# Kernel optimization log

Hardware: AMD Instinct MI355X
Metric: run time of the kernel (lower is better)

Reference implementation:

```python
import jax, jax.numpy as jnp
import numpy as np

NEG_SLOPE = 0.2
EPS = 1e-16  # PyG softmax denominator epsilon


def gatv2_layer(x, src, dst, W_l, W_r, att, bias, num_nodes, heads, out_dim, concat):
    # x: [N, F_in]; src/dst: [E] (self-loops already included)
    x_l = (x @ W_l).reshape(num_nodes, heads, out_dim)  # source transform
    x_r = (x @ W_r).reshape(num_nodes, heads, out_dim)  # target transform
    # GATv2 scoring: a^T LeakyReLU(x_l[j] + x_r[i])
    e = jax.nn.leaky_relu(x_l[src] + x_r[dst], NEG_SLOPE)       # [E, H, D]
    logits = jnp.einsum('ehd,hd->eh', e, att)                    # [E, H]
    # segment softmax over incoming edges of each target node
    m = jax.ops.segment_max(logits, dst, num_segments=num_nodes)  # [N, H]
    ex = jnp.exp(logits - m[dst])                                 # [E, H]
    denom = jax.ops.segment_sum(ex, dst, num_segments=num_nodes)  # [N, H]
    alpha = ex / (denom[dst] + EPS)                               # [E, H]
    msg = x_l[src] * alpha[:, :, None]                            # [E, H, D]
    out = jax.ops.segment_sum(msg, dst, num_segments=num_nodes)   # [N, H, D]
    if concat:
        out = out.reshape(num_nodes, heads * out_dim)
    else:
        out = out.mean(axis=1)
    return out + bias


def setup_inputs() -> dict:
    key = jax.random.key(0)
    ks = jax.random.split(key, 10)
    N, E, F_in, H, D, F_out = 50000, 400000, 256, 4, 128, 64

    def glorot(k, shape, fan):
        return jax.random.normal(k, shape, dtype=jnp.float32) * (1.0 / np.sqrt(fan))

    return {
        'x': jax.random.normal(ks[0], (N, F_in), dtype=jnp.float32),
        'edge_index': jax.random.randint(ks[1], (2, E), 0, N, dtype=jnp.int64),
        'W_l1': glorot(ks[2], (F_in, H * D), F_in),
        'W_r1': glorot(ks[3], (F_in, H * D), F_in),
        'att1': glorot(ks[4], (H, D), D),
        'b1': jnp.zeros((H * D,), dtype=jnp.float32),
        'W_l2': glorot(ks[5], (H * D, F_out), H * D),
        'W_r2': glorot(ks[6], (H * D, F_out), H * D),
        'att2': glorot(ks[7], (1, F_out), F_out),
        'b2': jnp.zeros((F_out,), dtype=jnp.float32),
    }


def reference(x, edge_index, W_l1, W_r1, att1, b1, W_l2, W_r2, att2, b2):
    N = x.shape[0]
    # add self-loops (PyG GATv2Conv default add_self_loops=True)
    loops = jnp.arange(N, dtype=edge_index.dtype)
    src = jnp.concatenate([edge_index[0], loops])
    dst = jnp.concatenate([edge_index[1], loops])
    # dropout(p=0.6) is identity in eval mode
    h = gatv2_layer(x, src, dst, W_l1, W_r1, att1, b1, N, heads=4, out_dim=128, concat=True)
    h = jax.nn.elu(h)
    out = gatv2_layer(h, src, dst, W_l2, W_r2, att2, b2, N, heads=1, out_dim=64, concat=False)
    return out
```

## Files before the change

### kernel.cpp

```cpp
#include <hip/hip_runtime.h>
#include <hip/hip_bf16.h>
#include <math.h>


#define NEG_SLOPE 0.2f
#define LOG2E 1.4426950408889634f

typedef _Float16 half8 __attribute__((ext_vector_type(8)));
typedef _Float16 h2 __attribute__((ext_vector_type(2)));
typedef float f32x4 __attribute__((ext_vector_type(4)));
typedef float f32x2 __attribute__((ext_vector_type(2)));

#if __has_builtin(__builtin_amdgcn_global_load_lds)
#define HAS_GLL 1
__device__ __forceinline__ void gll16(const _Float16* g, _Float16* l) {
    __builtin_amdgcn_global_load_lds(
        (const __attribute__((address_space(1))) unsigned int*)g,
        (__attribute__((address_space(3))) unsigned int*)l, 16, 0, 0);
}
#endif

__device__ __forceinline__ float dot2acc(h2 a, h2 b, float c) {
#if __has_builtin(__builtin_amdgcn_fdot2)
    return __builtin_amdgcn_fdot2(a, b, c, false);
#else
    return fmaf((float)a[1], (float)b[1], fmaf((float)a[0], (float)b[0], c));
#endif
}

__device__ __forceinline__ float fast_exp2(float p) {
#if __has_builtin(__builtin_amdgcn_exp2f)
    return __builtin_amdgcn_exp2f(p);
#else
    return exp2f(p);
#endif
}


__global__ __launch_bounds__(256) void k_castx_count(const float* __restrict__ x, _Float16* __restrict__ xh,
                                                     int n8, const int* __restrict__ ei,
                                                     int* __restrict__ counts, int E, int Etot, int gEtot) {
    int b = blockIdx.x;
    if (b < gEtot) {
        int i = b * 256 + threadIdx.x;
        if (i < Etot) {
            int dst = (i < E) ? ei[E + i] : (i - E);
            atomicAdd(&counts[dst], 1);
        }
    } else {
        int i = (b - gEtot) * 256 + threadIdx.x;
        if (i < n8) {
            const float4* p = (const float4*)(x + i * 8);
            float4 a = p[0], c = p[1];
            half8 v;
            v[0] = (_Float16)a.x; v[1] = (_Float16)a.y; v[2] = (_Float16)a.z; v[3] = (_Float16)a.w;
            v[4] = (_Float16)c.x; v[5] = (_Float16)c.y; v[6] = (_Float16)c.z; v[7] = (_Float16)c.w;
            *(half8*)(xh + i * 8) = v;
        }
    }
}


__global__ __launch_bounds__(1024) void k_castw_scana(const int* __restrict__ counts, int* __restrict__ offs,
                                                      int* __restrict__ partial, int n, int nsb,
                                                      const float* __restrict__ Wl1, const float* __restrict__ Wr1,
                                                      const float* __restrict__ Wl2, const float* __restrict__ Wr2,
                                                      _Float16* __restrict__ W1T, _Float16* __restrict__ W2T) {
    __shared__ int buf[1024];
    int b = blockIdx.x, t = threadIdx.x;
    if (b < nsb) {
        int i = b * 1024 + t;
        int v = (i < n) ? counts[i] : 0;
        buf[t] = v;
        __syncthreads();
        #pragma unroll
        for (int off = 1; off < 1024; off <<= 1) {
            int add = (t >= off) ? buf[t - off] : 0;
            __syncthreads();
            buf[t] += add;
            __syncthreads();
        }
        if (i < n) offs[i + 1] = buf[t];
        if (t == 1023) partial[b] = buf[1023];
    } else {
        int i = (b - nsb) * 1024 + t;
        const int T1 = 1024 * 256;
        const int T2 = 128 * 512;
        if (i < T1) {
            int nn = i >> 8, k = i & 255;
            float v = (nn < 512) ? Wl1[k * 512 + nn] : Wr1[k * 512 + (nn - 512)];
            W1T[i] = (_Float16)v;
        } else if (i < T1 + T2) {
            int j = i - T1;
            int nn = j >> 9, k = j & 511;
            float v = (nn < 64) ? Wl2[k * 64 + nn] : Wr2[k * 64 + (nn - 64)];
            W2T[j] = (_Float16)v;
        }
    }
}


__global__ __launch_bounds__(256) void k_scanbc(int* __restrict__ offs, int* __restrict__ cursor,
                                                const int* __restrict__ partial, int n, int nsb) {
    __shared__ int s[256];
    int t = threadIdx.x;
    int v = (t < nsb) ? partial[t] : 0;
    s[t] = v;
    __syncthreads();
    #pragma unroll
    for (int off = 1; off < 256; off <<= 1) {
        int add = (t >= off) ? s[t - off] : 0;
        __syncthreads();
        s[t] += add;
        __syncthreads();
    }
    int excl = s[t] - v;
    s[t] = excl;
    __syncthreads();
    int i = blockIdx.x * 256 + t;
    if (i == 0) { offs[0] = 0; cursor[0] = 0; }
    if (i < n) {
        int w = offs[i + 1] + s[i >> 10];
        offs[i + 1] = w;
        cursor[i + 1] = w;
    }
}


__device__ __forceinline__ void gemm_body(const _Float16* __restrict__ A,
                                          const _Float16* __restrict__ Bt,
                                          _Float16* __restrict__ C,
                                          int M, int N, int K, int ntiles, int blk,
                                          _Float16* As, _Float16* Bs) {
    int tid = threadIdx.x;
    int lane = tid & 63;
    int wave = tid >> 6;
    int wm = wave >> 2, wn = wave & 3;
    int l15 = lane & 15, q = lane >> 4;

    int ntile = blk % ntiles;
    int mtile = blk / ntiles;
    int tileM = mtile * 128;
    int tileN = ntile * 128;

    int srow = lane >> 2;
    int schunk = (lane & 3) ^ ((lane >> 3) & 3);
    const _Float16* gA = A + (long)(tileM + wave * 16 + srow) * K + schunk * 8;
    const _Float16* gB = Bt + (long)(tileN + wave * 16 + srow) * K + schunk * 8;
    _Float16* lA = As + wave * 512;
    _Float16* lB = Bs + wave * 512;

    int aswz = (q ^ ((l15 >> 1) & 3)) * 8;

    f32x4 acc[4][2];
    #pragma unroll
    for (int i = 0; i < 4; ++i)
        #pragma unroll
        for (int j = 0; j < 2; ++j)
            acc[i][j] = (f32x4)(0.f);

    for (int k0 = 0; k0 < K; k0 += 32) {
#ifdef HAS_GLL
        gll16(gA + k0, lA);
        gll16(gB + k0, lB);
#else
        half8 va = *(const half8*)(gA + k0);
        half8 vb = *(const half8*)(gB + k0);
        *(half8*)(lA + lane * 8) = va;
        *(half8*)(lB + lane * 8) = vb;
#endif
        __syncthreads();

        half8 af[4], bf[2];
        #pragma unroll
        for (int i = 0; i < 4; ++i)
            af[i] = *(const half8*)(As + (wm * 64 + i * 16 + l15) * 32 + aswz);
        #pragma unroll
        for (int j = 0; j < 2; ++j)
            bf[j] = *(const half8*)(Bs + (wn * 32 + j * 16 + l15) * 32 + aswz);
        #pragma unroll
        for (int i = 0; i < 4; ++i)
            #pragma unroll
            for (int j = 0; j < 2; ++j)
                acc[i][j] = __builtin_amdgcn_mfma_f32_16x16x32_f16(af[i], bf[j], acc[i][j], 0, 0, 0);
        __syncthreads();
    }

    #pragma unroll
    for (int i = 0; i < 4; ++i) {
        #pragma unroll
        for (int r = 0; r < 4; ++r) {
            int grow = tileM + wm * 64 + i * 16 + q * 4 + r;
            if (grow < M) {
                #pragma unroll
                for (int j = 0; j < 2; ++j) {
                    int gcol = tileN + wn * 32 + j * 16 + l15;
                    C[(long)grow * N + gcol] = (_Float16)acc[i][j][r];
                }
            }
        }
    }
}

__global__ __launch_bounds__(512) void k_gemm1_fill(const _Float16* __restrict__ A,
                                                    const _Float16* __restrict__ Bt,
                                                    _Float16* __restrict__ C,
                                                    int M, int N, int K, int ntiles, int gb,
                                                    const int* __restrict__ ei, int* __restrict__ cursor,
                                                    int* __restrict__ csr_src, int E, int Etot) {
    __shared__ _Float16 As[128 * 32];
    __shared__ _Float16 Bs[128 * 32];
    int b = blockIdx.x;
    if (b < gb) {
        gemm_body(A, Bt, C, M, N, K, ntiles, b, As, Bs);
    } else {
        int i = (b - gb) * 512 + threadIdx.x;
        if (i < Etot) {
            int src, dst;
            if (i < E) { src = ei[i]; dst = ei[E + i]; }
            else       { src = i - E; dst = i - E; }
            int pos = atomicAdd(&cursor[dst], 1);
            csr_src[pos] = src;
        }
    }
}

__global__ __launch_bounds__(512) void k_gemm_f16(const _Float16* __restrict__ A,
                                                  const _Float16* __restrict__ Bt,
                                                  _Float16* __restrict__ C,
                                                  int M, int N, int K, int ntiles) {
    __shared__ _Float16 As[128 * 32];
    __shared__ _Float16 Bs[128 * 32];
    gemm_body(A, Bt, C, M, N, K, ntiles, blockIdx.x, As, Bs);
}


__global__ __launch_bounds__(256) void k_attn1(const _Float16* __restrict__ xlr,
                                               const float* __restrict__ att, const float* __restrict__ b1,
                                               const int* __restrict__ offs, const int* __restrict__ csr_src,
                                               _Float16* __restrict__ hout, int N) {
    int wave = threadIdx.x >> 6;
    int lane = threadIdx.x & 63;
    int node = blockIdx.x * 4 + wave;
    if (node >= N) return;

    int cbase = (lane >> 4) * 128 + (lane & 15) * 8;
    const _Float16* xlr_l = xlr + cbase;

    half8 xrv8 = *(const half8*)(xlr_l + ((unsigned)node << 10) + 512);
    float4 atv0 = *(const float4*)(att + cbase);
    float4 atv1 = *(const float4*)(att + cbase + 4);
    h2 xr[4], at[4];
    #pragma unroll
    for (int j = 0; j < 4; ++j) {
        xr[j][0] = xrv8[2 * j]; xr[j][1] = xrv8[2 * j + 1];
    }
    at[0][0] = (_Float16)(atv0.x * LOG2E); at[0][1] = (_Float16)(atv0.y * LOG2E);
    at[1][0] = (_Float16)(atv0.z * LOG2E); at[1][1] = (_Float16)(atv0.w * LOG2E);
    at[2][0] = (_Float16)(atv1.x * LOG2E); at[2][1] = (_Float16)(atv1.y * LOG2E);
    at[3][0] = (_Float16)(atv1.z * LOG2E); at[3][1] = (_Float16)(atv1.w * LOG2E);
    const h2 ns2 = {(_Float16)NEG_SLOPE, (_Float16)NEG_SLOPE};

    float l = 0.f;
    f32x2 acc[4];
    #pragma unroll
    for (int j = 0; j < 4; ++j) acc[j] = (f32x2)(0.f);

    int e0 = offs[node], e1 = offs[node + 1];
    int s_next = csr_src[e0];
    int s_next2 = (e0 + 1 < e1) ? csr_src[e0 + 1] : 0;
    half8 xlv = *(const half8*)(xlr_l + ((unsigned)s_next << 10));

    for (int e = e0; e < e1; ++e) {
        half8 cur = xlv;
        int s_pf = s_next2;
        if (e + 2 < e1) s_next2 = csr_src[e + 2];
        if (e + 1 < e1) xlv = *(const half8*)(xlr_l + ((unsigned)s_pf << 10));

        const h2* cp = (const h2*)&cur;
        float p = 0.f;
        #pragma unroll
        for (int j = 0; j < 4; ++j) {
            h2 t = cp[j] + xr[j];
#if __has_builtin(__builtin_elementwise_max)
            t = __builtin_elementwise_max(t, t * ns2);
#else
            h2 tn = t * ns2;
            t[0] = (t[0] > tn[0]) ? t[0] : tn[0];
            t[1] = (t[1] > tn[1]) ? t[1] : tn[1];
#endif
            p = dot2acc(t, at[j], p);
        }
        #pragma unroll
        for (int off = 1; off <= 8; off <<= 1) p += __shfl_xor(p, off, 64);
        float w = fast_exp2(p);
        l += w;
        f32x2 w2 = {w, w};
        #pragma unroll
        for (int j = 0; j < 4; ++j) {
            f32x2 xf = {(float)cur[2 * j], (float)cur[2 * j + 1]};
            acc[j] = w2 * xf + acc[j];
        }
    }

    float inv = 1.f / (l + 1e-16f);
    float4 b1v0 = *(const float4*)(b1 + cbase);
    float4 b1v1 = *(const float4*)(b1 + cbase + 4);
    float bb[8] = {b1v0.x, b1v0.y, b1v0.z, b1v0.w, b1v1.x, b1v1.y, b1v1.z, b1v1.w};
    half8 ov;
    #pragma unroll
    for (int j = 0; j < 8; ++j) {
        float o = fmaf(acc[j >> 1][j & 1], inv, bb[j]);
        o = (o > 0.f) ? o : (__expf(o) - 1.f);
        ov[j] = (_Float16)o;
    }
    *(half8*)(hout + (long)node * 512 + cbase) = ov;
}


__global__ __launch_bounds__(256) void k_attn2(const _Float16* __restrict__ xlr2,
                                               const float* __restrict__ att, const float* __restrict__ b2,
                                               const int* __restrict__ offs, const int* __restrict__ csr_src,
                                               float* __restrict__ out, int N) {
    int wave = threadIdx.x >> 6;
    int lane = threadIdx.x & 63;
    int node = blockIdx.x * 4 + wave;
    if (node >= N) return;

    int eh = lane >> 5;
    int hl = lane & 31;
    int ch = hl * 2;
    const _Float16* xlr_l = xlr2 + ch;

    h2 xrh = *(const h2*)(xlr_l + ((unsigned)node << 7) + 64);
    float2 atf = *(const float2*)(att + ch);
    h2 ath; ath[0] = (_Float16)(atf.x * LOG2E); ath[1] = (_Float16)(atf.y * LOG2E);
    const h2 ns2 = {(_Float16)NEG_SLOPE, (_Float16)NEG_SLOPE};

    float l = 0.f;
    f32x2 acc = (f32x2)(0.f);
    int e0 = offs[node], e1 = offs[node + 1];
    int e = e0 + eh;
    h2 cv;
    if (e < e1) {
        int s = csr_src[e];
        cv = *(const h2*)(xlr_l + ((unsigned)s << 7));
    }
    while (e < e1) {
        h2 u = cv;
        int en = e + 2;
        if (en < e1) {
            int s = csr_src[en];
            cv = *(const h2*)(xlr_l + ((unsigned)s << 7));
        }
        h2 t = u + xrh;
#if __has_builtin(__builtin_elementwise_max)
        t = __builtin_elementwise_max(t, t * ns2);
#else
        h2 tn = t * ns2;
        t[0] = (t[0] > tn[0]) ? t[0] : tn[0];
        t[1] = (t[1] > tn[1]) ? t[1] : tn[1];
#endif
        float p = dot2acc(t, ath, 0.f);
        p += __shfl_xor(p, 1, 64);
        p += __shfl_xor(p, 2, 64);
        p += __shfl_xor(p, 4, 64);
        p += __shfl_xor(p, 8, 64);
        p += __shfl_xor(p, 16, 64);
        float w = fast_exp2(p);
        l += w;
        f32x2 w2 = {w, w};
        f32x2 xf = {(float)u[0], (float)u[1]};
        acc = w2 * xf + acc;
        e = en;
    }
    l += __shfl_xor(l, 32, 64);
    acc[0] += __shfl_xor(acc[0], 32, 64);
    acc[1] += __shfl_xor(acc[1], 32, 64);
    if (eh == 0) {
        float inv = 1.f / (l + 1e-16f);
        float2 o;
        o.x = fmaf(acc[0], inv, b2[ch]);
        o.y = fmaf(acc[1], inv, b2[ch + 1]);
        *(float2*)(out + (long)node * 64 + ch) = o;
    }
}


extern "C" void kernel_launch(void* const* d_in, const int* in_sizes, int n_in,
                              void* d_out, int out_size, void* d_ws, size_t ws_size,
                              hipStream_t stream) {
    const float* x    = (const float*)d_in[0];
    const int*   ei   = (const int*)d_in[1];
    const float* Wl1  = (const float*)d_in[2];
    const float* Wr1  = (const float*)d_in[3];
    const float* att1 = (const float*)d_in[4];
    const float* b1   = (const float*)d_in[5];
    const float* Wl2  = (const float*)d_in[6];
    const float* Wr2  = (const float*)d_in[7];
    const float* att2 = (const float*)d_in[8];
    const float* b2   = (const float*)d_in[9];
    float* out = (float*)d_out;

    const int F_IN = 256;
    int N = in_sizes[0] / F_IN;
    int E = in_sizes[1] / 2;
    int Etot = E + N;
    int nScanBlocks = (N + 1023) / 1024;
    int mtiles = (N + 127) / 128;
    int Mpad = mtiles * 128;

    char* p = (char*)d_ws;
    auto carve = [&](size_t bytes) -> void* {
        void* r = (void*)p;
        p += (bytes + 255) & ~(size_t)255;
        return r;
    };
    _Float16* xh   = (_Float16*)carve((size_t)Mpad * 256 * 2);
    _Float16* W1T  = (_Float16*)carve((size_t)1024 * 256 * 2);
    _Float16* W2T  = (_Float16*)carve((size_t)128 * 512 * 2);
    _Float16* C1   = (_Float16*)carve((size_t)N * 1024 * 2);
    _Float16* h    = (_Float16*)carve((size_t)Mpad * 512 * 2);
    _Float16* C2   = (_Float16*)carve((size_t)N * 128 * 2);
    int* counts  = (int*)carve((size_t)N * 4);
    int* offs    = (int*)carve((size_t)(N + 1) * 4);
    int* cursor  = (int*)carve((size_t)(N + 1) * 4);
    int* partial = (int*)carve((size_t)nScanBlocks * 4);
    int* csr     = (int*)carve((size_t)Etot * 4);

    int gN    = (N + 255) / 256;
    int gEtot = (Etot + 255) / 256;
    int n8    = N * 256 / 8;
    int gCast = (n8 + 255) / 256;

    hipMemsetAsync(counts, 0, (size_t)N * 4, stream);

    k_castx_count<<<gEtot + gCast, 256, 0, stream>>>(x, xh, n8, ei, counts, E, Etot, gEtot);

    {
        int total = 1024 * 256 + 128 * 512;
        int gW = (total + 1023) / 1024;
        k_castw_scana<<<nScanBlocks + gW, 1024, 0, stream>>>(counts, offs, partial, N, nScanBlocks,
                                                             Wl1, Wr1, Wl2, Wr2, W1T, W2T);
    }
    k_scanbc<<<gN, 256, 0, stream>>>(offs, cursor, partial, N, nScanBlocks);

    {
        int gb = mtiles * 8;
        int fillBlocks = (Etot + 511) / 512;
        k_gemm1_fill<<<gb + fillBlocks, 512, 0, stream>>>(xh, W1T, C1, N, 1024, 256, 8, gb,
                                                          ei, cursor, csr, E, Etot);
    }
    k_attn1<<<(N + 3) / 4, 256, 0, stream>>>(C1, att1, b1, offs, csr, h, N);

    k_gemm_f16<<<mtiles, 512, 0, stream>>>(h, W2T, C2, N, 128, 512, 1);
    k_attn2<<<(N + 3) / 4, 256, 0, stream>>>(C2, att2, b2, offs, csr, out, N);
}
```

Measured before the change: 325.4 us.

## Split layer-1 projections into separate buffers and process two edges per wave

The first GEMM now writes the source and target projections into two separate contiguous N×512 buffers instead of one interleaved N×1024 buffer, so gathered source rows are packed more densely. The layer-1 attention kernel is restructured so each half-wave handles alternate edges, with each lane covering 16 channels. The two halves' partial sums are combined by a cross-half shuffle at the end. The aim is more memory-level parallelism in the edge gather and fewer serial loop iterations, at the cost of more registers, extra reductions, and idle lanes when a node's degree is odd.

Result: slower. 333.1 us (+2.4%).

```diff
diff --git a/kernel.cpp b/kernel.cpp
--- a/kernel.cpp
+++ b/kernel.cpp
@@ -129,7 +129,8 @@
 
 __device__ __forceinline__ void gemm_body(const _Float16* __restrict__ A,
                                           const _Float16* __restrict__ Bt,
-                                          _Float16* __restrict__ C,
+                                          _Float16* __restrict__ CA,
+                                          _Float16* __restrict__ CB, int S,
                                           int M, int N, int K, int ntiles, int blk,
                                           _Float16* As, _Float16* Bs) {
     int tid = threadIdx.x;
@@ -195,7 +196,9 @@
                 #pragma unroll
                 for (int j = 0; j < 2; ++j) {
                     int gcol = tileN + wn * 32 + j * 16 + l15;
-                    C[(long)grow * N + gcol] = (_Float16)acc[i][j][r];
+                    _Float16 val = (_Float16)acc[i][j][r];
+                    if (gcol < S) CA[(long)grow * S + gcol] = val;
+                    else          CB[(long)grow * S + gcol - S] = val;
                 }
             }
         }
@@ -204,7 +207,8 @@
 
 __global__ __launch_bounds__(512) void k_gemm1_fill(const _Float16* __restrict__ A,
                                                     const _Float16* __restrict__ Bt,
-                                                    _Float16* __restrict__ C,
+                                                    _Float16* __restrict__ CA,
+                                                    _Float16* __restrict__ CB, int S,
                                                     int M, int N, int K, int ntiles, int gb,
                                                     const int* __restrict__ ei, int* __restrict__ cursor,
                                                     int* __restrict__ csr_src, int E, int Etot) {
@@ -212,7 +216,7 @@
     __shared__ _Float16 Bs[128 * 32];
     int b = blockIdx.x;
     if (b < gb) {
-        gemm_body(A, Bt, C, M, N, K, ntiles, b, As, Bs);
+        gemm_body(A, Bt, CA, CB, S, M, N, K, ntiles, b, As, Bs);
     } else {
         int i = (b - gb) * 512 + threadIdx.x;
         if (i < Etot) {
@@ -231,11 +235,12 @@
                                                   int M, int N, int K, int ntiles) {
     __shared__ _Float16 As[128 * 32];
     __shared__ _Float16 Bs[128 * 32];
-    gemm_body(A, Bt, C, M, N, K, ntiles, blockIdx.x, As, Bs);
-}
-
-
-__global__ __launch_bounds__(256) void k_attn1(const _Float16* __restrict__ xlr,
+    gemm_body(A, Bt, C, C, N, M, N, K, ntiles, blockIdx.x, As, Bs);
+}
+
+
+__global__ __launch_bounds__(256) void k_attn1(const _Float16* __restrict__ xl,
+                                               const _Float16* __restrict__ xrp,
                                                const float* __restrict__ att, const float* __restrict__ b1,
                                                const int* __restrict__ offs, const int* __restrict__ csr_src,
                                                _Float16* __restrict__ hout, int N) {
@@ -244,44 +249,59 @@
     int node = blockIdx.x * 4 + wave;
     if (node >= N) return;
 
-    int cbase = (lane >> 4) * 128 + (lane & 15) * 8;
-    const _Float16* xlr_l = xlr + cbase;
-
-    half8 xrv8 = *(const half8*)(xlr_l + ((unsigned)node << 10) + 512);
-    float4 atv0 = *(const float4*)(att + cbase);
-    float4 atv1 = *(const float4*)(att + cbase + 4);
-    h2 xr[4], at[4];
+    int eh = lane >> 5;
+    int hl = lane & 31;
+    int cbase = (hl >> 3) * 128 + (hl & 7) * 16;
+    const _Float16* xl_l = xl + cbase;
+
+    half8 xr0 = *(const half8*)(xrp + (unsigned)node * 512u + cbase);
+    half8 xr1 = *(const half8*)(xrp + (unsigned)node * 512u + cbase + 8);
+
+    float4 a0 = *(const float4*)(att + cbase);
+    float4 a1 = *(const float4*)(att + cbase + 4);
+    float4 a2 = *(const float4*)(att + cbase + 8);
+    float4 a3 = *(const float4*)(att + cbase + 12);
+    h2 at[8];
+    at[0][0] = (_Float16)(a0.x * LOG2E); at[0][1] = (_Float16)(a0.y * LOG2E);
+    at[1][0] = (_Float16)(a0.z * LOG2E); at[1][1] = (_Float16)(a0.w * LOG2E);
+    at[2][0] = (_Float16)(a1.x * LOG2E); at[2][1] = (_Float16)(a1.y * LOG2E);
+    at[3][0] = (_Float16)(a1.z * LOG2E); at[3][1] = (_Float16)(a1.w * LOG2E);
+    at[4][0] = (_Float16)(a2.x * LOG2E); at[4][1] = (_Float16)(a2.y * LOG2E);
+    at[5][0] = (_Float16)(a2.z * LOG2E); at[5][1] = (_Float16)(a2.w * LOG2E);
+    at[6][0] = (_Float16)(a3.x * LOG2E); at[6][1] = (_Float16)(a3.y * LOG2E);
+    at[7][0] = (_Float16)(a3.z * LOG2E); at[7][1] = (_Float16)(a3.w * LOG2E);
+    const h2 ns2 = {(_Float16)NEG_SLOPE, (_Float16)NEG_SLOPE};
+
+    float l = 0.f;
+    float acc[16];
     #pragma unroll
-    for (int j = 0; j < 4; ++j) {
-        xr[j][0] = xrv8[2 * j]; xr[j][1] = xrv8[2 * j + 1];
-    }
-    at[0][0] = (_Float16)(atv0.x * LOG2E); at[0][1] = (_Float16)(atv0.y * LOG2E);
-    at[1][0] = (_Float16)(atv0.z * LOG2E); at[1][1] = (_Float16)(atv0.w * LOG2E);
-    at[2][0] = (_Float16)(atv1.x * LOG2E); at[2][1] = (_Float16)(atv1.y * LOG2E);
-    at[3][0] = (_Float16)(atv1.z * LOG2E); at[3][1] = (_Float16)(atv1.w * LOG2E);
-    const h2 ns2 = {(_Float16)NEG_SLOPE, (_Float16)NEG_SLOPE};
-
-    float l = 0.f;
-    f32x2 acc[4];
-    #pragma unroll
-    for (int j = 0; j < 4; ++j) acc[j] = (f32x2)(0.f);
+    for (int j = 0; j < 16; ++j) acc[j] = 0.f;
 
     int e0 = offs[node], e1 = offs[node + 1];
-    int s_next = csr_src[e0];
-    int s_next2 = (e0 + 1 < e1) ? csr_src[e0 + 1] : 0;
-    half8 xlv = *(const half8*)(xlr_l + ((unsigned)s_next << 10));
-
-    for (int e = e0; e < e1; ++e) {
-        half8 cur = xlv;
-        int s_pf = s_next2;
-        if (e + 2 < e1) s_next2 = csr_src[e + 2];
-        if (e + 1 < e1) xlv = *(const half8*)(xlr_l + ((unsigned)s_pf << 10));
-
-        const h2* cp = (const h2*)&cur;
+    int e = e0 + eh;
+    half8 c0, c1;
+    if (e < e1) {
+        unsigned ro = (unsigned)csr_src[e] << 9;
+        c0 = *(const half8*)(xl_l + ro);
+        c1 = *(const half8*)(xl_l + ro + 8);
+    }
+    while (e < e1) {
+        half8 u0 = c0, u1 = c1;
+        int en = e + 2;
+        if (en < e1) {
+            unsigned ro = (unsigned)csr_src[en] << 9;
+            c0 = *(const half8*)(xl_l + ro);
+            c1 = *(const half8*)(xl_l + ro + 8);
+        }
+
+        const h2* up0 = (const h2*)&u0;
+        const h2* up1 = (const h2*)&u1;
+        const h2* xp0 = (const h2*)&xr0;
+        const h2* xp1 = (const h2*)&xr1;
         float p = 0.f;
         #pragma unroll
         for (int j = 0; j < 4; ++j) {
-            h2 t = cp[j] + xr[j];
+            h2 t = up0[j] + xp0[j];
 #if __has_builtin(__builtin_elementwise_max)
             t = __builtin_elementwise_max(t, t * ns2);
 #else
@@ -292,29 +312,57 @@
             p = dot2acc(t, at[j], p);
         }
         #pragma unroll
-        for (int off = 1; off <= 8; off <<= 1) p += __shfl_xor(p, off, 64);
+        for (int j = 0; j < 4; ++j) {
+            h2 t = up1[j] + xp1[j];
+#if __has_builtin(__builtin_elementwise_max)
+            t = __builtin_elementwise_max(t, t * ns2);
+#else
+            h2 tn = t * ns2;
+            t[0] = (t[0] > tn[0]) ? t[0] : tn[0];
+            t[1] = (t[1] > tn[1]) ? t[1] : tn[1];
+#endif
+            p = dot2acc(t, at[4 + j], p);
+        }
+        p += __shfl_xor(p, 1, 64);
+        p += __shfl_xor(p, 2, 64);
+        p += __shfl_xor(p, 4, 64);
         float w = fast_exp2(p);
         l += w;
-        f32x2 w2 = {w, w};
-        #pragma unroll
-        for (int j = 0; j < 4; ++j) {
-            f32x2 xf = {(float)cur[2 * j], (float)cur[2 * j + 1]};
-            acc[j] = w2 * xf + acc[j];
-        }
-    }
-
-    float inv = 1.f / (l + 1e-16f);
-    float4 b1v0 = *(const float4*)(b1 + cbase);
-    float4 b1v1 = *(const float4*)(b1 + cbase + 4);
-    float bb[8] = {b1v0.x, b1v0.y, b1v0.z, b1v0.w, b1v1.x, b1v1.y, b1v1.z, b1v1.w};
-    half8 ov;
+        #pragma unroll
+        for (int j = 0; j < 8; ++j) acc[j]     = fmaf((float)u0[j], w, acc[j]);
+        #pragma unroll
+        for (int j = 0; j < 8; ++j) acc[8 + j] = fmaf((float)u1[j], w, acc[8 + j]);
+        e = en;
+    }
+
+    l += __shfl_xor(l, 32, 64);
     #pragma unroll
-    for (int j = 0; j < 8; ++j) {
-        float o = fmaf(acc[j >> 1][j & 1], inv, bb[j]);
-        o = (o > 0.f) ? o : (__expf(o) - 1.f);
-        ov[j] = (_Float16)o;
-    }
-    *(half8*)(hout + (long)node * 512 + cbase) = ov;
+    for (int j = 0; j < 16; ++j) acc[j] += __shfl_xor(acc[j], 32, 64);
+
+    if (eh == 0) {
+        float inv = 1.f / (l + 1e-16f);
+        float4 b0 = *(const float4*)(b1 + cbase);
+        float4 bsecond = *(const float4*)(b1 + cbase + 4);
+        float4 b2q = *(const float4*)(b1 + cbase + 8);
+        float4 b3q = *(const float4*)(b1 + cbase + 12);
+        float bb[16] = {b0.x, b0.y, b0.z, b0.w, bsecond.x, bsecond.y, bsecond.z, bsecond.w,
+                        b2q.x, b2q.y, b2q.z, b2q.w, b3q.x, b3q.y, b3q.z, b3q.w};
+        half8 ov0, ov1;
+        #pragma unroll
+        for (int j = 0; j < 8; ++j) {
+            float o = fmaf(acc[j], inv, bb[j]);
+            o = (o > 0.f) ? o : (__expf(o) - 1.f);
+            ov0[j] = (_Float16)o;
+        }
+        #pragma unroll
+        for (int j = 0; j < 8; ++j) {
+            float o = fmaf(acc[8 + j], inv, bb[8 + j]);
+            o = (o > 0.f) ? o : (__expf(o) - 1.f);
+            ov1[j] = (_Float16)o;
+        }
+        *(half8*)(hout + (long)node * 512 + cbase) = ov0;
+        *(half8*)(hout + (long)node * 512 + cbase + 8) = ov1;
+    }
 }
 
 
@@ -419,7 +467,8 @@
     _Float16* xh   = (_Float16*)carve((size_t)Mpad * 256 * 2);
     _Float16* W1T  = (_Float16*)carve((size_t)1024 * 256 * 2);
     _Float16* W2T  = (_Float16*)carve((size_t)128 * 512 * 2);
-    _Float16* C1   = (_Float16*)carve((size_t)N * 1024 * 2);
+    _Float16* C1L  = (_Float16*)carve((size_t)N * 512 * 2);
+    _Float16* C1R  = (_Float16*)carve((size_t)N * 512 * 2);
     _Float16* h    = (_Float16*)carve((size_t)Mpad * 512 * 2);
     _Float16* C2   = (_Float16*)carve((size_t)N * 128 * 2);
     int* counts  = (int*)carve((size_t)N * 4);
@@ -448,10 +497,11 @@
     {
         int gb = mtiles * 8;
         int fillBlocks = (Etot + 511) / 512;
-        k_gemm1_fill<<<gb + fillBlocks, 512, 0, stream>>>(xh, W1T, C1, N, 1024, 256, 8, gb,
+        k_gemm1_fill<<<gb + fillBlocks, 512, 0, stream>>>(xh, W1T, C1L, C1R, 512,
+                                                          N, 1024, 256, 8, gb,
                                                           ei, cursor, csr, E, Etot);
     }
-    k_attn1<<<(N + 3) / 4, 256, 0, stream>>>(C1, att1, b1, offs, csr, h, N);
+    k_attn1<<<(N + 3) / 4, 256, 0, stream>>>(C1L, C1R, att1, b1, offs, csr, h, N);
 
     k_gemm_f16<<<mtiles, 512, 0, stream>>>(h, W2T, C2, N, 128, 512, 1);
     k_attn2<<<(N + 3) / 4, 256, 0, stream>>>(C2, att2, b2, offs, csr, out, N);
```

## Split layer-1 attention into one wave per node-head with DPP reductions

Applied to the files above, without the earlier changes.

The layer-1 attention kernel now gives each node-head pair its own wave, so each lane handles 2 channels instead of 8. Launch size grows fourfold through a head index taken from the block id. The per-edge 16-lane logit reduction now uses DPP row ops plus two cross-row shuffles instead of four shuffles, and the result is summed across the whole 64-lane head. This adds parallelism and latency hiding for the gather-bound loop. In exchange, each wave issues narrow 4-byte gathers and repeats the CSR index loads and exp work four times per node.

Measured after the change: 432.9 us. +33.0%, slower.

```diff
diff --git a/kernel.cpp b/kernel.cpp
--- a/kernel.cpp
+++ b/kernel.cpp
@@ -34,6 +34,21 @@
 #else
     return exp2f(p);
 #endif
+}
+
+
+template <int CTRL>
+__device__ __forceinline__ float dpp_addf(float x) {
+    int y = __builtin_amdgcn_update_dpp(0, __builtin_bit_cast(int, x), CTRL, 0xF, 0xF, true);
+    return x + __builtin_bit_cast(float, y);
+}
+
+__device__ __forceinline__ float row16_sum(float x) {
+    x = dpp_addf<0xB1>(x);
+    x = dpp_addf<0x4E>(x);
+    x = dpp_addf<0x124>(x);
+    x = dpp_addf<0x128>(x);
+    return x;
 }
 
 
@@ -241,80 +256,58 @@
                                                _Float16* __restrict__ hout, int N) {
     int wave = threadIdx.x >> 6;
     int lane = threadIdx.x & 63;
-    int node = blockIdx.x * 4 + wave;
+    int head = blockIdx.x & 3;
+    int node = (blockIdx.x >> 2) * 4 + wave;
     if (node >= N) return;
 
-    int cbase = (lane >> 4) * 128 + (lane & 15) * 8;
-    const _Float16* xlr_l = xlr + cbase;
-
-    half8 xrv8 = *(const half8*)(xlr_l + ((unsigned)node << 10) + 512);
-    float4 atv0 = *(const float4*)(att + cbase);
-    float4 atv1 = *(const float4*)(att + cbase + 4);
-    h2 xr[4], at[4];
-    #pragma unroll
-    for (int j = 0; j < 4; ++j) {
-        xr[j][0] = xrv8[2 * j]; xr[j][1] = xrv8[2 * j + 1];
-    }
-    at[0][0] = (_Float16)(atv0.x * LOG2E); at[0][1] = (_Float16)(atv0.y * LOG2E);
-    at[1][0] = (_Float16)(atv0.z * LOG2E); at[1][1] = (_Float16)(atv0.w * LOG2E);
-    at[2][0] = (_Float16)(atv1.x * LOG2E); at[2][1] = (_Float16)(atv1.y * LOG2E);
-    at[3][0] = (_Float16)(atv1.z * LOG2E); at[3][1] = (_Float16)(atv1.w * LOG2E);
+    int col = head * 128 + lane * 2;
+    const _Float16* xlr_l = xlr + col;
+
+    h2 xrh = *(const h2*)(xlr_l + ((unsigned)node << 10) + 512);
+    float2 atf = *(const float2*)(att + col);
+    h2 ath; ath[0] = (_Float16)(atf.x * LOG2E); ath[1] = (_Float16)(atf.y * LOG2E);
     const h2 ns2 = {(_Float16)NEG_SLOPE, (_Float16)NEG_SLOPE};
 
     float l = 0.f;
-    f32x2 acc[4];
-    #pragma unroll
-    for (int j = 0; j < 4; ++j) acc[j] = (f32x2)(0.f);
+    float acc0 = 0.f, acc1 = 0.f;
 
     int e0 = offs[node], e1 = offs[node + 1];
     int s_next = csr_src[e0];
     int s_next2 = (e0 + 1 < e1) ? csr_src[e0 + 1] : 0;
-    half8 xlv = *(const half8*)(xlr_l + ((unsigned)s_next << 10));
+    h2 xlv = *(const h2*)(xlr_l + ((unsigned)s_next << 10));
 
     for (int e = e0; e < e1; ++e) {
-        half8 cur = xlv;
+        h2 cur = xlv;
         int s_pf = s_next2;
         if (e + 2 < e1) s_next2 = csr_src[e + 2];
-        if (e + 1 < e1) xlv = *(const half8*)(xlr_l + ((unsigned)s_pf << 10));
-
-        const h2* cp = (const h2*)&cur;
-        float p = 0.f;
-        #pragma unroll
-        for (int j = 0; j < 4; ++j) {
-            h2 t = cp[j] + xr[j];
+        if (e + 1 < e1) xlv = *(const h2*)(xlr_l + ((unsigned)s_pf << 10));
+
+        h2 t = cur + xrh;
 #if __has_builtin(__builtin_elementwise_max)
-            t = __builtin_elementwise_max(t, t * ns2);
+        t = __builtin_elementwise_max(t, t * ns2);
 #else
-            h2 tn = t * ns2;
-            t[0] = (t[0] > tn[0]) ? t[0] : tn[0];
-            t[1] = (t[1] > tn[1]) ? t[1] : tn[1];
-#endif
-            p = dot2acc(t, at[j], p);
-        }
-        #pragma unroll
-        for (int off = 1; off <= 8; off <<= 1) p += __shfl_xor(p, off, 64);
+        h2 tn = t * ns2;
+        t[0] = (t[0] > tn[0]) ? t[0] : tn[0];
+        t[1] = (t[1] > tn[1]) ? t[1] : tn[1];
+#endif
+        float p = dot2acc(t, ath, 0.f);
+        p = row16_sum(p);
+        p += __shfl_xor(p, 16, 64);
+        p += __shfl_xor(p, 32, 64);
         float w = fast_exp2(p);
         l += w;
-        f32x2 w2 = {w, w};
-        #pragma unroll
-        for (int j = 0; j < 4; ++j) {
-            f32x2 xf = {(float)cur[2 * j], (float)cur[2 * j + 1]};
-            acc[j] = w2 * xf + acc[j];
-        }
+        acc0 = fmaf((float)cur[0], w, acc0);
+        acc1 = fmaf((float)cur[1], w, acc1);
     }
 
     float inv = 1.f / (l + 1e-16f);
-    float4 b1v0 = *(const float4*)(b1 + cbase);
-    float4 b1v1 = *(const float4*)(b1 + cbase + 4);
-    float bb[8] = {b1v0.x, b1v0.y, b1v0.z, b1v0.w, b1v1.x, b1v1.y, b1v1.z, b1v1.w};
-    half8 ov;
-    #pragma unroll
-    for (int j = 0; j < 8; ++j) {
-        float o = fmaf(acc[j >> 1][j & 1], inv, bb[j]);
-        o = (o > 0.f) ? o : (__expf(o) - 1.f);
-        ov[j] = (_Float16)o;
-    }
-    *(half8*)(hout + (long)node * 512 + cbase) = ov;
+    float2 bf = *(const float2*)(b1 + col);
+    float o0 = fmaf(acc0, inv, bf.x);
+    float o1 = fmaf(acc1, inv, bf.y);
+    o0 = (o0 > 0.f) ? o0 : (__expf(o0) - 1.f);
+    o1 = (o1 > 0.f) ? o1 : (__expf(o1) - 1.f);
+    h2 ov; ov[0] = (_Float16)o0; ov[1] = (_Float16)o1;
+    *(h2*)(hout + (long)node * 512 + col) = ov;
 }
 
 
@@ -451,7 +444,10 @@
         k_gemm1_fill<<<gb + fillBlocks, 512, 0, stream>>>(xh, W1T, C1, N, 1024, 256, 8, gb,
                                                           ei, cursor, csr, E, Etot);
     }
-    k_attn1<<<(N + 3) / 4, 256, 0, stream>>>(C1, att1, b1, offs, csr, h, N);
+    {
+        int nb = ((N + 3) / 4) * 4;
+        k_attn1<<<nb, 256, 0, stream>>>(C1, att1, b1, offs, csr, h, N);
+    }
 
     k_gemm_f16<<<mtiles, 512, 0, stream>>>(h, W2T, C2, N, 128, 512, 1);
     k_attn2<<<(N + 3) / 4, 256, 0, stream>>>(C2, att2, b2, offs, csr, out, N);
```
